# Kernel optimization log

Measured on AMD Instinct MI355X. Metric: run time of the kernel, lower is better.

The kernel has to match this reference:

```python
import jax, jax.numpy as jnp
import numpy as np

V, E = 50000, 300          # vocab, embedding dim (Word2Vec)
U1, U2, DNS = 256, 256, 128  # lstm1 units, lstm2 units, dense units
B, S = 64, 512             # batch, seq_len


def _glorot(key, shape):
    fan_in, fan_out = shape
    lim = jnp.sqrt(6.0 / (fan_in + fan_out))
    return jax.random.uniform(key, shape, jnp.float32, -lim, lim)


def setup_inputs() -> dict:
    key = jax.random.key(0)
    ks = jax.random.split(key, 12)
    d = {
        'tokens': jax.random.randint(ks[0], (B, S), 0, V),
        'emb': jax.random.normal(ks[1], (V, E), jnp.float32) * 0.05,
        # layer 1 gates: combined dim = E + U1
        'W1f': _glorot(ks[2], (E + U1, U1)), 'b1f': jnp.zeros((U1,), jnp.float32),
        'W1i': _glorot(ks[3], (E + U1, U1)), 'b1i': jnp.zeros((U1,), jnp.float32),
        'W1c': _glorot(ks[4], (E + U1, U1)), 'b1c': jnp.zeros((U1,), jnp.float32),
        'W1o': _glorot(ks[5], (E + U1, U1)), 'b1o': jnp.zeros((U1,), jnp.float32),
        # layer 2 gates: combined dim = U1 + U2
        'W2f': _glorot(ks[6], (U1 + U2, U2)), 'b2f': jnp.zeros((U2,), jnp.float32),
        'W2i': _glorot(ks[7], (U1 + U2, U2)), 'b2i': jnp.zeros((U2,), jnp.float32),
        'W2c': _glorot(ks[8], (U1 + U2, U2)), 'b2c': jnp.zeros((U2,), jnp.float32),
        'W2o': _glorot(ks[9], (U1 + U2, U2)), 'b2o': jnp.zeros((U2,), jnp.float32),
        'Wd': _glorot(ks[10], (U2, DNS)), 'bd': jnp.zeros((DNS,), jnp.float32),
        'Wout': _glorot(ks[11], (DNS, 1)), 'bout': jnp.zeros((1,), jnp.float32),
    }
    return d


def _lstm(x_seq, Wf, bf, Wi, bi, Wc, bc, Wo, bo, units):
    # x_seq: [B, S, D]; scan over time, returns all hidden states [B, S, units]
    b = x_seq.shape[0]
    h0 = jnp.zeros((b, units), x_seq.dtype)
    c0 = jnp.zeros((b, units), x_seq.dtype)

    def step(carry, x_t):
        h, c = carry
        z = jnp.concatenate([x_t, h], axis=-1)           # [B, D+units]
        f = jax.nn.sigmoid(z @ Wf + bf)
        i = jax.nn.sigmoid(z @ Wi + bi)
        g = jnp.tanh(z @ Wc + bc)
        c_new = f * c + i * g
        o = jax.nn.sigmoid(z @ Wo + bo)
        h_new = o * jnp.tanh(c_new)
        return (h_new, c_new), h_new

    (_, _), hs = jax.lax.scan(step, (h0, c0), jnp.swapaxes(x_seq, 0, 1))
    return jnp.swapaxes(hs, 0, 1)  # [B, S, units]


def reference(tokens, emb, W1f, b1f, W1i, b1i, W1c, b1c, W1o, b1o,
              W2f, b2f, W2i, b2i, W2c, b2c, W2o, b2o, Wd, bd, Wout, bout):
    x = emb[tokens]                                       # [B, S, E]
    h1 = _lstm(x, W1f, b1f, W1i, b1i, W1c, b1c, W1o, b1o, U1)   # [B, S, U1]
    h2 = _lstm(h1, W2f, b2f, W2i, b2i, W2c, b2c, W2o, b2o, U2)  # [B, S, U2]
    last = h2[:, -1, :]                                   # return_sequences=False -> final h
    d = jax.nn.relu(last @ Wd + bd)
    return jax.nn.sigmoid(d @ Wout + bout)                # [B, 1]
```

## Files before the change

kernel.cpp:

```cpp
#include <hip/hip_runtime.h>
#include <stdint.h>

typedef __bf16 bf16_t;
typedef __bf16 bf16x8 __attribute__((ext_vector_type(8)));
typedef float floatx16 __attribute__((ext_vector_type(16)));
typedef unsigned int u32;
typedef unsigned long long u64;

#define NPROD 64
#define H1R   8
#define SST   592
#define ZST   1104
#define FP    32

struct KParams {
  const int* tok;
  const float* emb;
  const float* W1[4]; const float* b1[4];
  const float* W2[4]; const float* b2[4];
  const float* Wd; const float* bd; const float* Wout; const float* bout;
  float* out;
  uint16_t* h1;
  uint16_t* h2;
  u32* fl0;
  u32* fl1;
  u32* fl0g;
  u32* pflags;
  float* dstage;
  bf16_t* w1bf;
  float* gx;
  int R;
};

__device__ __forceinline__ float sigf(float x) { return 1.f / (1.f + __expf(-x)); }
__device__ __forceinline__ float tanhf_fast(float x) { return 1.f - 2.f / (__expf(2.f * x) + 1.f); }

__device__ __forceinline__ u32 pack2(float a, float b) {
  uint16_t x = __builtin_bit_cast(uint16_t, (bf16_t)a);
  uint16_t y = __builtin_bit_cast(uint16_t, (bf16_t)b);
  return ((u32)y << 16) | (u32)x;
}
__device__ __forceinline__ float2 u2f2(u64 v) { union { u64 u; float2 f; } x; x.u = v; return x.f; }

__device__ __forceinline__ u32  ald32(const u32* p) { return __hip_atomic_load(p, __ATOMIC_RELAXED, __HIP_MEMORY_SCOPE_AGENT); }
__device__ __forceinline__ void ast32(u32* p, u32 v) { __hip_atomic_store(p, v, __ATOMIC_RELAXED, __HIP_MEMORY_SCOPE_AGENT); }
__device__ __forceinline__ u64  ald64(const u64* p) { return __hip_atomic_load(p, __ATOMIC_RELAXED, __HIP_MEMORY_SCOPE_AGENT); }

template<int NA, int NB>
__device__ __forceinline__ void waitcond(const u32* fa, u32 na, const u32* fb, u32 nb,
                                         const u32* pc, u32 nc) {
  const int lane = threadIdx.x & 63;
  const u32* ap; u32 need;
  if (lane < NA)           { ap = fa + lane * FP;        need = na; }
  else if (lane < NA + NB) { ap = fb + (lane - NA) * FP; need = nb; }
  else                     { ap = pc;                    need = nc; }
  while (!__all(ald32(ap) >= need)) {}
  __atomic_signal_fence(__ATOMIC_ACQUIRE);
}

__device__ __forceinline__ void waitg16(const u32* fa, u32 na) {
  const int lane = threadIdx.x & 63;
  const u32* ap = fa + (lane & 15) * FP;
  while (!__all(ald32(ap) >= na)) {}
  __atomic_signal_fence(__ATOMIC_ACQUIRE);
}

__device__ __forceinline__ void stage_h64(const u64* hp, char* smem) {
  const int tid = threadIdx.x;
  u64 tmp[16];
#pragma unroll
  for (int t = 0; t < 16; ++t) tmp[t] = ald64(hp + tid + 256 * t);
#pragma unroll
  for (int t = 0; t < 16; ++t) {
    int i = tid + 256 * t, b = i >> 6, cc = i & 63;
    *(u64*)(smem + b * SST + cc * 8) = tmp[t];
  }
}

__device__ void run_l0(const KParams& p, int sub, char* abuf, float* cst, float* biasl)
{
  const int tid = threadIdx.x;
  const int w = tid >> 6, l = tid & 63, q = l >> 5, lr = l & 31;
  const int mh = w & 1, nh = w >> 1;

  if (tid < 64) biasl[tid] = p.b1[tid >> 4][sub * 16 + (tid & 15)];

  const int c = nh * 32 + lr;
  const float* Wg = p.W1[c >> 4];
  const int un = sub * 16 + (c & 15);
  bf16x8 wf[16];
#pragma unroll
  for (int s = 0; s < 16; ++s)
#pragma unroll
    for (int j = 0; j < 8; ++j) {
      int k = 16 * s + 8 * q + j;
      wf[s][j] = (bf16_t)Wg[(300 + k) * 256 + un];
    }
  __syncthreads();

  float cs[2][2] = {{0.f, 0.f}, {0.f, 0.f}};

  for (int s = 0; s < 512; ++s) {
    u32 n1 = (s >= 8) ? (u32)(s - 7) : 0u;
    if (w == 0) waitcond<16, 32>(p.fl0, (u32)s, p.fl1, n1, &p.pflags[s * FP], 1u);
    __syncthreads();

    const float* slab = p.gx + (size_t)(s % p.R) * 65536u;
    u64 g[2][4];
#pragma unroll
    for (int kk = 0; kk < 2; ++kk) {
      int pp = tid + 256 * kk, b = pp >> 3, u2 = (pp & 7) * 2;
      const float* gb = slab + b * 1024 + sub * 64 + u2;
      g[kk][0] = ald64((const u64*)gb);
      g[kk][1] = ald64((const u64*)(gb + 16));
      g[kk][2] = ald64((const u64*)(gb + 32));
      g[kk][3] = ald64((const u64*)(gb + 48));
    }
    stage_h64((const u64*)(p.h1 + ((s + H1R - 1) & (H1R - 1)) * 16384), abuf);
    __syncthreads();

    floatx16 acc;
#pragma unroll
    for (int e = 0; e < 16; ++e) acc[e] = 0.f;
    const char* arow = abuf + (mh * 32 + lr) * SST + q * 16;
#pragma unroll
    for (int s2 = 0; s2 < 16; ++s2) {
      bf16x8 af = *(const bf16x8*)(arow + 32 * s2);
      acc = __builtin_amdgcn_mfma_f32_32x32x16_bf16(af, wf[s2], acc, 0, 0, 0);
    }
#pragma unroll
    for (int e = 0; e < 16; ++e) {
      int ri = (e & 3) + 8 * (e >> 2) + 4 * q;
      cst[(mh * 32 + ri) * 68 + nh * 32 + lr] = acc[e];
    }
    __syncthreads();

    uint16_t* hout = p.h1 + (s & (H1R - 1)) * 16384;
#pragma unroll
    for (int kk = 0; kk < 2; ++kk) {
      int pp = tid + 256 * kk, b = pp >> 3, u2 = (pp & 7) * 2;
      float2 pf = *(float2*)&cst[b * 68 +      u2];
      float2 pi = *(float2*)&cst[b * 68 + 16 + u2];
      float2 pg = *(float2*)&cst[b * 68 + 32 + u2];
      float2 po = *(float2*)&cst[b * 68 + 48 + u2];
      float2 gf = u2f2(g[kk][0]), gi = u2f2(g[kk][1]);
      float2 gg = u2f2(g[kk][2]), go = u2f2(g[kk][3]);
      float hv[2];
#pragma unroll
      for (int j = 0; j < 2; ++j) {
        float fj = sigf((j ? pf.y : pf.x) + (j ? gf.y : gf.x) + biasl[u2 + j]);
        float ij = sigf((j ? pi.y : pi.x) + (j ? gi.y : gi.x) + biasl[16 + u2 + j]);
        float gj = tanhf_fast((j ? pg.y : pg.x) + (j ? gg.y : gg.x) + biasl[32 + u2 + j]);
        float oj = sigf((j ? po.y : po.x) + (j ? go.y : go.x) + biasl[48 + u2 + j]);
        float cn = fj * cs[kk][j] + ij * gj;
        cs[kk][j] = cn;
        hv[j] = oj * tanhf_fast(cn);
      }
      ast32((u32*)(hout + b * 256 + sub * 16 + u2), pack2(hv[0], hv[1]));
    }
    __syncthreads();
    if (tid == 0) {
      ast32(&p.fl0[sub * FP], (u32)(s + 1));
      ast32(&p.fl0g[sub * FP], (u32)(s + 1));
    }
  }
}

__device__ void run_l1(const KParams& p, int w2, char* zbuf, float* cst, float* biasl)
{
  const int tid = threadIdx.x;
  const int wv = tid >> 6, l = tid & 63, q = l >> 5, lr = l & 31;
  const int nh = wv & 1, kh = wv >> 1;
  const int bh = w2 & 1, sub1 = w2 >> 1;

  if (tid < 64) biasl[tid] = p.b2[tid >> 4][sub1 * 16 + (tid & 15)];

  const int c = nh * 32 + lr;
  const float* Wg = p.W2[c >> 4];
  const int un = sub1 * 16 + (c & 15);
  bf16x8 wf[16];
#pragma unroll
  for (int s = 0; s < 16; ++s)
#pragma unroll
    for (int j = 0; j < 8; ++j) {
      int k = kh * 256 + s * 16 + q * 8 + j;
      wf[s][j] = (bf16_t)Wg[k * 256 + un];
    }
  __syncthreads();

  float cs2[2] = {0.f, 0.f};
  const int cb = tid >> 3, cu = (tid & 7) * 2;

  for (int s = 0; s < 512; ++s) {
    if (wv == 0) waitcond<32, 16>(p.fl1, (u32)s, p.fl0, (u32)(s + 1), p.fl0, 0u);
    __syncthreads();

    const u64* hp1 = (const u64*)(p.h1 + (s & (H1R - 1)) * 16384) + bh * 2048;
    const u64* hp2 = (const u64*)(p.h2 + ((s + 1) & 1) * 16384) + bh * 2048;
    u64 t1[8], t2[8];
#pragma unroll
    for (int t = 0; t < 8; ++t) t1[t] = ald64(hp1 + tid + 256 * t);
#pragma unroll
    for (int t = 0; t < 8; ++t) t2[t] = ald64(hp2 + tid + 256 * t);
#pragma unroll
    for (int t = 0; t < 8; ++t) {
      int i = tid + 256 * t, r = i >> 6, cc = i & 63;
      *(u64*)(zbuf + r * ZST + cc * 8) = t1[t];
    }
#pragma unroll
    for (int t = 0; t < 8; ++t) {
      int i = tid + 256 * t, r = i >> 6, cc = i & 63;
      *(u64*)(zbuf + r * ZST + 512 + cc * 8) = t2[t];
    }
    __syncthreads();

    floatx16 acc;
#pragma unroll
    for (int e = 0; e < 16; ++e) acc[e] = 0.f;
    const char* arow = zbuf + lr * ZST + kh * 512 + q * 16;
#pragma unroll
    for (int s2 = 0; s2 < 16; ++s2) {
      bf16x8 af = *(const bf16x8*)(arow + 32 * s2);
      acc = __builtin_amdgcn_mfma_f32_32x32x16_bf16(af, wf[s2], acc, 0, 0, 0);
    }
#pragma unroll
    for (int e = 0; e < 16; ++e) {
      int ri = (e & 3) + 8 * (e >> 2) + 4 * q;
      cst[kh * 2176 + ri * 68 + nh * 32 + lr] = acc[e];
    }
    __syncthreads();

    uint16_t* hout = p.h2 + (s & 1) * 16384;
    {
      float2 pf = *(float2*)&cst[cb * 68 +      cu];
      float2 pi = *(float2*)&cst[cb * 68 + 16 + cu];
      float2 pg = *(float2*)&cst[cb * 68 + 32 + cu];
      float2 po = *(float2*)&cst[cb * 68 + 48 + cu];
      float2 qf = *(float2*)&cst[2176 + cb * 68 +      cu];
      float2 qi = *(float2*)&cst[2176 + cb * 68 + 16 + cu];
      float2 qg = *(float2*)&cst[2176 + cb * 68 + 32 + cu];
      float2 qo = *(float2*)&cst[2176 + cb * 68 + 48 + cu];
      float hv[2];
#pragma unroll
      for (int j = 0; j < 2; ++j) {
        float fj = sigf((j ? pf.y + qf.y : pf.x + qf.x) + biasl[cu + j]);
        float ij = sigf((j ? pi.y + qi.y : pi.x + qi.x) + biasl[16 + cu + j]);
        float gj = tanhf_fast((j ? pg.y + qg.y : pg.x + qg.x) + biasl[32 + cu + j]);
        float oj = sigf((j ? po.y + qo.y : po.x + qo.x) + biasl[48 + cu + j]);
        float cn = fj * cs2[j] + ij * gj;
        cs2[j] = cn;
        hv[j] = oj * tanhf_fast(cn);
      }
      ast32((u32*)(hout + (bh * 32 + cb) * 256 + sub1 * 16 + cu), pack2(hv[0], hv[1]));
    }
    __syncthreads();
    if (tid == 0) ast32(&p.fl1[w2 * FP], (u32)(s + 1));
  }

  if (wv == 0) waitcond<32, 0>(p.fl1, 512u, p.fl1, 0u, p.fl1, 0u);
  __syncthreads();
  {
    const u64* hp = (const u64*)(p.h2 + 16384);
    u64 tmp[16];
#pragma unroll
    for (int t = 0; t < 16; ++t) tmp[t] = ald64(hp + tid + 256 * t);
#pragma unroll
    for (int t = 0; t < 16; ++t) {
      int i = tid + 256 * t, b = i >> 6, cc = i & 63;
      *(u64*)(zbuf + b * 520 + cc * 8) = tmp[t];
    }
  }
  __syncthreads();
  {
    int b = tid >> 2, cc = w2 * 4 + (tid & 3);
    const bf16_t* hrow = (const bf16_t*)(zbuf + b * 520);
    float a = p.bd[cc];
#pragma unroll 8
    for (int k = 0; k < 256; ++k) a += (float)hrow[k] * p.Wd[k * 128 + cc];
    ast32((u32*)&p.dstage[b * 128 + cc], __builtin_bit_cast(u32, fmaxf(a, 0.f)));
  }
  __syncthreads();
  if (tid == 0) ast32(&p.fl1[w2 * FP], 513u);

  if (w2 == 0) {
    if (wv == 0) waitcond<32, 0>(p.fl1, 513u, p.fl1, 0u, p.fl1, 0u);
    __syncthreads();
    if (tid < 64) {
      float a = p.bout[0];
#pragma unroll 8
      for (int cc = 0; cc < 128; ++cc) {
        u32 dv = ald32((u32*)&p.dstage[tid * 128 + cc]);
        a += __builtin_bit_cast(float, dv) * p.Wout[cc];
      }
      p.out[tid] = sigf(a);
    }
  }
}

__device__ void run_prod(const KParams& p, int pw, char* smem)
{
  const int tid = threadIdx.x;
  const int w = tid >> 6, l = tid & 63, q = l >> 5, lr = l & 31;
  const int mh = w & 1, chalf = w >> 1;
  const int R = p.R;

  for (int jj = 0; jj < 512 / NPROD; ++jj) {
    const int s = pw + NPROD * jj;
    if (s >= R) {
      if (w == 0) waitg16(p.fl0g, (u32)(s - R + 1));
    }
    __syncthreads();
    {
      int b = tid >> 2, qq = tid & 3;
      int tokv = p.tok[b * 512 + s];
      const float4* src = (const float4*)(p.emb + (size_t)tokv * 300);
      char* dst = smem + b * 656;
      for (int j2 = qq; j2 < 75; j2 += 4) {
        float4 v = src[j2];
        *(u32*)(dst + 8 * j2)     = pack2(v.x, v.y);
        *(u32*)(dst + 8 * j2 + 4) = pack2(v.z, v.w);
      }
      for (int i = tid; i < 640; i += 256) {
        int bb = i / 10, cc2 = i % 10;
        *(u32*)(smem + bb * 656 + 600 + cc2 * 4) = 0u;
      }
    }
    __syncthreads();

    bf16x8 afr[20];
    const char* arow = smem + (mh * 32 + lr) * 656 + q * 16;
#pragma unroll
    for (int kt = 0; kt < 20; ++kt) afr[kt] = *(const bf16x8*)(arow + 32 * kt);

    float* slab = p.gx + (size_t)(s % R) * 65536u;
    for (int c2 = 0; c2 < 16; ++c2) {
      int n = (chalf * 16 + c2) * 32 + lr;
      floatx16 acc;
#pragma unroll
      for (int e = 0; e < 16; ++e) acc[e] = 0.f;
#pragma unroll
      for (int kt = 0; kt < 20; ++kt) {
        bf16x8 bf = ((const bf16x8*)p.w1bf)[(kt * 1024 + n) * 2 + q];
        acc = __builtin_amdgcn_mfma_f32_32x32x16_bf16(afr[kt], bf, acc, 0, 0, 0);
      }
#pragma unroll
      for (int e = 0; e < 16; ++e) {
        int ri = (e & 3) + 8 * (e >> 2) + 4 * q;
        ast32((u32*)(slab + (mh * 32 + ri) * 1024 + n), __builtin_bit_cast(u32, acc[e]));
      }
    }
    __syncthreads();
    if (tid == 0) ast32(&p.pflags[s * FP], 1u);
  }
}

__global__ __launch_bounds__(256, 1) void lstm_main(KParams p)
{
  __shared__ __align__(16) char smem[64 * 656];
  __shared__ float cst[4352];
  __shared__ float biasl[64];
  const int wg = blockIdx.x;
  if (wg < 16)       run_l0(p, wg, smem, cst, biasl);
  else if (wg < 48)  run_l1(p, wg - 16, smem, cst, biasl);
  else               run_prod(p, wg - 48, smem);
}

__global__ void prep_w(KParams p) {
  int idx = blockIdx.x * 256 + threadIdx.x;
  if (idx >= 20 * 1024 * 16) return;
  int kk = idx & 15, n = (idx >> 4) & 1023, kt = idx >> 14;
  int k = kt * 16 + kk;
  int g = (n >> 4) & 3, su = n >> 6, u = n & 15;
  float v = (k < 300) ? p.W1[g][k * 256 + su * 16 + u] : 0.f;
  p.w1bf[idx] = (bf16_t)v;
}

__global__ void init_ws(u32* ws32) {
  int i = blockIdx.x * 256 + threadIdx.x;
  if (i < 100352) ws32[i] = 0u;
}

extern "C" void kernel_launch(void* const* d_in, const int* in_sizes, int n_in,
                              void* d_out, int out_size, void* d_ws, size_t ws_size,
                              hipStream_t stream)
{
  KParams p;
  p.tok = (const int*)d_in[0];
  p.emb = (const float*)d_in[1];
  for (int g = 0; g < 4; ++g) {
    p.W1[g] = (const float*)d_in[2 + 2 * g];
    p.b1[g] = (const float*)d_in[3 + 2 * g];
    p.W2[g] = (const float*)d_in[10 + 2 * g];
    p.b2[g] = (const float*)d_in[11 + 2 * g];
  }
  p.Wd   = (const float*)d_in[18];
  p.bd   = (const float*)d_in[19];
  p.Wout = (const float*)d_in[20];
  p.bout = (const float*)d_in[21];
  p.out  = (float*)d_out;

  char* ws = (char*)d_ws;
  p.h1     = (uint16_t*)ws;
  p.h2     = (uint16_t*)(ws + 262144);
  p.fl0    = (u32*)(ws + 327680);
  p.fl1    = (u32*)(ws + 329728);
  p.fl0g   = (u32*)(ws + 333824);
  p.pflags = (u32*)(ws + 335872);
  p.dstage = (float*)(ws + 401408);
  p.w1bf   = (bf16_t*)(ws + 434176);
  p.gx     = (float*)(ws + 1089536);

  long avail = (long)ws_size - 1089536L;
  int R = (int)(avail / 262144L);
  if (R > 64) R = 64;
  if (R < 1)  R = 1;
  p.R = R;

  hipLaunchKernelGGL(init_ws, dim3(392), dim3(256), 0, stream, (u32*)d_ws);
  hipLaunchKernelGGL(prep_w, dim3(1280), dim3(256), 0, stream, p);
  hipLaunchKernelGGL(lstm_main, dim3(16 + 32 + NPROD), dim3(256), 0, stream, p);
}
```

Before: 1.860 ms.

## Split LSTM batch into two halves and software-pipeline recurrence phases

Each layer's persistent workgroups now process the batch as two 32-row halves in alternating phases. While one half runs its MFMA and gate math, the hidden-state and gate-input loads for the other half are prefetched into registers, and the flag polling overlaps the MFMA work. Layer-1 is re-split so each workgroup owns 8 units across 4 K-slices with a cross-wave reduction, and per-half flags plus a larger h1 ring are added. This aims to hide global-memory latency and synchronisation on the serial recurrence critical path. The cost is more flags, more register pressure and more complex dependency tracking.

```diff
diff --git a/kernel.cpp b/kernel.cpp
--- a/kernel.cpp
+++ b/kernel.cpp
@@ -8,10 +8,12 @@
 typedef unsigned long long u64;
 
 #define NPROD 64
-#define H1R   8
+#define H1R   16
 #define SST   592
 #define ZST   1104
 #define FP    32
+
+template<int V> struct IC { static constexpr int value = V; };
 
 struct KParams {
   const int* tok;
@@ -65,161 +67,71 @@
   __atomic_signal_fence(__ATOMIC_ACQUIRE);
 }
 
-__device__ __forceinline__ void stage_h64(const u64* hp, char* smem) {
-  const int tid = threadIdx.x;
-  u64 tmp[16];
-#pragma unroll
-  for (int t = 0; t < 16; ++t) tmp[t] = ald64(hp + tid + 256 * t);
-#pragma unroll
-  for (int t = 0; t < 16; ++t) {
-    int i = tid + 256 * t, b = i >> 6, cc = i & 63;
-    *(u64*)(smem + b * SST + cc * 8) = tmp[t];
-  }
-}
-
 __device__ void run_l0(const KParams& p, int sub, char* abuf, float* cst, float* biasl)
 {
   const int tid = threadIdx.x;
   const int w = tid >> 6, l = tid & 63, q = l >> 5, lr = l & 31;
-  const int mh = w & 1, nh = w >> 1;
+  const int nh = w & 1, kh = w >> 1;
+  const int b2 = tid >> 3, u2 = (tid & 7) * 2;
 
   if (tid < 64) biasl[tid] = p.b1[tid >> 4][sub * 16 + (tid & 15)];
 
   const int c = nh * 32 + lr;
   const float* Wg = p.W1[c >> 4];
   const int un = sub * 16 + (c & 15);
-  bf16x8 wf[16];
-#pragma unroll
-  for (int s = 0; s < 16; ++s)
+  bf16x8 wf[8];
+#pragma unroll
+  for (int s2 = 0; s2 < 8; ++s2)
 #pragma unroll
     for (int j = 0; j < 8; ++j) {
-      int k = 16 * s + 8 * q + j;
-      wf[s][j] = (bf16_t)Wg[(300 + k) * 256 + un];
-    }
+      int k = kh * 128 + 16 * s2 + 8 * q + j;
+      wf[s2][j] = (bf16_t)Wg[(300 + k) * 256 + un];
+    }
+
+  float csA[2] = {0.f, 0.f}, csB[2] = {0.f, 0.f};
+  u64 rH[8], rG[4], rHn[8], rGn[4];
+
+  if (w == 0) waitcond<16, 32>(p.fl0, 0u, p.fl1, 0u, &p.pflags[0], 1u);
   __syncthreads();
-
-  float cs[2][2] = {{0.f, 0.f}, {0.f, 0.f}};
-
-  for (int s = 0; s < 512; ++s) {
-    u32 n1 = (s >= 8) ? (u32)(s - 7) : 0u;
-    if (w == 0) waitcond<16, 32>(p.fl0, (u32)s, p.fl1, n1, &p.pflags[s * FP], 1u);
-    __syncthreads();
-
-    const float* slab = p.gx + (size_t)(s % p.R) * 65536u;
-    u64 g[2][4];
-#pragma unroll
-    for (int kk = 0; kk < 2; ++kk) {
-      int pp = tid + 256 * kk, b = pp >> 3, u2 = (pp & 7) * 2;
-      const float* gb = slab + b * 1024 + sub * 64 + u2;
-      g[kk][0] = ald64((const u64*)gb);
-      g[kk][1] = ald64((const u64*)(gb + 16));
-      g[kk][2] = ald64((const u64*)(gb + 32));
-      g[kk][3] = ald64((const u64*)(gb + 48));
-    }
-    stage_h64((const u64*)(p.h1 + ((s + H1R - 1) & (H1R - 1)) * 16384), abuf);
-    __syncthreads();
-
-    floatx16 acc;
-#pragma unroll
-    for (int e = 0; e < 16; ++e) acc[e] = 0.f;
-    const char* arow = abuf + (mh * 32 + lr) * SST + q * 16;
-#pragma unroll
-    for (int s2 = 0; s2 < 16; ++s2) {
-      bf16x8 af = *(const bf16x8*)(arow + 32 * s2);
-      acc = __builtin_amdgcn_mfma_f32_32x32x16_bf16(af, wf[s2], acc, 0, 0, 0);
-    }
-#pragma unroll
-    for (int e = 0; e < 16; ++e) {
-      int ri = (e & 3) + 8 * (e >> 2) + 4 * q;
-      cst[(mh * 32 + ri) * 68 + nh * 32 + lr] = acc[e];
-    }
-    __syncthreads();
-
-    uint16_t* hout = p.h1 + (s & (H1R - 1)) * 16384;
-#pragma unroll
-    for (int kk = 0; kk < 2; ++kk) {
-      int pp = tid + 256 * kk, b = pp >> 3, u2 = (pp & 7) * 2;
-      float2 pf = *(float2*)&cst[b * 68 +      u2];
-      float2 pi = *(float2*)&cst[b * 68 + 16 + u2];
-      float2 pg = *(float2*)&cst[b * 68 + 32 + u2];
-      float2 po = *(float2*)&cst[b * 68 + 48 + u2];
-      float2 gf = u2f2(g[kk][0]), gi = u2f2(g[kk][1]);
-      float2 gg = u2f2(g[kk][2]), go = u2f2(g[kk][3]);
-      float hv[2];
-#pragma unroll
-      for (int j = 0; j < 2; ++j) {
-        float fj = sigf((j ? pf.y : pf.x) + (j ? gf.y : gf.x) + biasl[u2 + j]);
-        float ij = sigf((j ? pi.y : pi.x) + (j ? gi.y : gi.x) + biasl[16 + u2 + j]);
-        float gj = tanhf_fast((j ? pg.y : pg.x) + (j ? gg.y : gg.x) + biasl[32 + u2 + j]);
-        float oj = sigf((j ? po.y : po.x) + (j ? go.y : go.x) + biasl[48 + u2 + j]);
-        float cn = fj * cs[kk][j] + ij * gj;
-        cs[kk][j] = cn;
-        hv[j] = oj * tanhf_fast(cn);
-      }
-      ast32((u32*)(hout + b * 256 + sub * 16 + u2), pack2(hv[0], hv[1]));
-    }
-    __syncthreads();
-    if (tid == 0) {
-      ast32(&p.fl0[sub * FP], (u32)(s + 1));
-      ast32(&p.fl0g[sub * FP], (u32)(s + 1));
-    }
-  }
-}
-
-__device__ void run_l1(const KParams& p, int w2, char* zbuf, float* cst, float* biasl)
-{
-  const int tid = threadIdx.x;
-  const int wv = tid >> 6, l = tid & 63, q = l >> 5, lr = l & 31;
-  const int nh = wv & 1, kh = wv >> 1;
-  const int bh = w2 & 1, sub1 = w2 >> 1;
-
-  if (tid < 64) biasl[tid] = p.b2[tid >> 4][sub1 * 16 + (tid & 15)];
-
-  const int c = nh * 32 + lr;
-  const float* Wg = p.W2[c >> 4];
-  const int un = sub1 * 16 + (c & 15);
-  bf16x8 wf[16];
-#pragma unroll
-  for (int s = 0; s < 16; ++s)
-#pragma unroll
-    for (int j = 0; j < 8; ++j) {
-      int k = kh * 256 + s * 16 + q * 8 + j;
-      wf[s][j] = (bf16_t)Wg[k * 256 + un];
-    }
-  __syncthreads();
-
-  float cs2[2] = {0.f, 0.f};
-  const int cb = tid >> 3, cu = (tid & 7) * 2;
-
-  for (int s = 0; s < 512; ++s) {
-    if (wv == 0) waitcond<32, 16>(p.fl1, (u32)s, p.fl0, (u32)(s + 1), p.fl0, 0u);
-    __syncthreads();
-
-    const u64* hp1 = (const u64*)(p.h1 + (s & (H1R - 1)) * 16384) + bh * 2048;
-    const u64* hp2 = (const u64*)(p.h2 + ((s + 1) & 1) * 16384) + bh * 2048;
-    u64 t1[8], t2[8];
-#pragma unroll
-    for (int t = 0; t < 8; ++t) t1[t] = ald64(hp1 + tid + 256 * t);
-#pragma unroll
-    for (int t = 0; t < 8; ++t) t2[t] = ald64(hp2 + tid + 256 * t);
+  {
+    const u64* hp = (const u64*)(p.h1 + (H1R - 1) * 16384);
+#pragma unroll
+    for (int t = 0; t < 8; ++t) rH[t] = ald64(hp + tid + 256 * t);
+    const float* gb = p.gx + (size_t)b2 * 1024 + sub * 64 + u2;
+    rG[0] = ald64((const u64*)gb);
+    rG[1] = ald64((const u64*)(gb + 16));
+    rG[2] = ald64((const u64*)(gb + 32));
+    rG[3] = ald64((const u64*)(gb + 48));
+  }
+
+  auto phase = [&](auto HC, int s) {
+    constexpr int h  = decltype(HC)::value;
+    constexpr int hn = 1 - h;
+    const int sn = h ? (s + 1) : s;
+    const bool haveNext = !(h == 1 && s == 511);
+
 #pragma unroll
     for (int t = 0; t < 8; ++t) {
       int i = tid + 256 * t, r = i >> 6, cc = i & 63;
-      *(u64*)(zbuf + r * ZST + cc * 8) = t1[t];
-    }
-#pragma unroll
-    for (int t = 0; t < 8; ++t) {
-      int i = tid + 256 * t, r = i >> 6, cc = i & 63;
-      *(u64*)(zbuf + r * ZST + 512 + cc * 8) = t2[t];
-    }
-    __syncthreads();
+      *(u64*)(abuf + r * SST + cc * 8) = rH[t];
+    }
+    __syncthreads();
+
+    const u32* pollp = &p.pflags[0]; u32 need = 0u, fpre = 1u;
+    if (w == 0 && haveNext) {
+      if (l < 16)      { pollp = p.fl0 + (hn * 16 + l) * FP;        need = (u32)sn; }
+      else if (l < 48) { pollp = p.fl1 + (hn * 32 + (l - 16)) * FP;
+                         need = (sn >= H1R) ? (u32)(sn - (H1R - 1)) : 0u; }
+      else             { pollp = &p.pflags[sn * FP];                need = 1u; }
+      fpre = ald32(pollp);
+    }
 
     floatx16 acc;
 #pragma unroll
     for (int e = 0; e < 16; ++e) acc[e] = 0.f;
-    const char* arow = zbuf + lr * ZST + kh * 512 + q * 16;
-#pragma unroll
-    for (int s2 = 0; s2 < 16; ++s2) {
+    const char* arow = abuf + lr * SST + kh * 256 + q * 16;
+#pragma unroll
+    for (int s2 = 0; s2 < 8; ++s2) {
       bf16x8 af = *(const bf16x8*)(arow + 32 * s2);
       acc = __builtin_amdgcn_mfma_f32_32x32x16_bf16(af, wf[s2], acc, 0, 0, 0);
     }
@@ -228,36 +140,194 @@
       int ri = (e & 3) + 8 * (e >> 2) + 4 * q;
       cst[kh * 2176 + ri * 68 + nh * 32 + lr] = acc[e];
     }
-    __syncthreads();
-
-    uint16_t* hout = p.h2 + (s & 1) * 16384;
+    if (w == 0 && haveNext) {
+      while (!__all(fpre >= need)) fpre = ald32(pollp);
+      __atomic_signal_fence(__ATOMIC_ACQUIRE);
+    }
+    __syncthreads();
+
+    if (haveNext) {
+      const u64* hp = (const u64*)(p.h1 + ((sn + H1R - 1) & (H1R - 1)) * 16384) + hn * 2048;
+#pragma unroll
+      for (int t = 0; t < 8; ++t) rHn[t] = ald64(hp + tid + 256 * t);
+      const float* gb = p.gx + (size_t)(sn % p.R) * 65536u + (hn * 32 + b2) * 1024 + sub * 64 + u2;
+      rGn[0] = ald64((const u64*)gb);
+      rGn[1] = ald64((const u64*)(gb + 16));
+      rGn[2] = ald64((const u64*)(gb + 32));
+      rGn[3] = ald64((const u64*)(gb + 48));
+    }
+
     {
-      float2 pf = *(float2*)&cst[cb * 68 +      cu];
-      float2 pi = *(float2*)&cst[cb * 68 + 16 + cu];
-      float2 pg = *(float2*)&cst[cb * 68 + 32 + cu];
-      float2 po = *(float2*)&cst[cb * 68 + 48 + cu];
-      float2 qf = *(float2*)&cst[2176 + cb * 68 +      cu];
-      float2 qi = *(float2*)&cst[2176 + cb * 68 + 16 + cu];
-      float2 qg = *(float2*)&cst[2176 + cb * 68 + 32 + cu];
-      float2 qo = *(float2*)&cst[2176 + cb * 68 + 48 + cu];
+      float2 gf = u2f2(rG[0]), gi = u2f2(rG[1]), gg = u2f2(rG[2]), go = u2f2(rG[3]);
+      const int base = b2 * 68 + u2;
+      float2 af0 = *(float2*)&cst[base],      af1 = *(float2*)&cst[2176 + base];
+      float2 ai0 = *(float2*)&cst[base + 16], ai1 = *(float2*)&cst[2176 + base + 16];
+      float2 ag0 = *(float2*)&cst[base + 32], ag1 = *(float2*)&cst[2176 + base + 32];
+      float2 ao0 = *(float2*)&cst[base + 48], ao1 = *(float2*)&cst[2176 + base + 48];
+      float csel[2] = { h ? csB[0] : csA[0], h ? csB[1] : csA[1] };
       float hv[2];
 #pragma unroll
       for (int j = 0; j < 2; ++j) {
-        float fj = sigf((j ? pf.y + qf.y : pf.x + qf.x) + biasl[cu + j]);
-        float ij = sigf((j ? pi.y + qi.y : pi.x + qi.x) + biasl[16 + cu + j]);
-        float gj = tanhf_fast((j ? pg.y + qg.y : pg.x + qg.x) + biasl[32 + cu + j]);
-        float oj = sigf((j ? po.y + qo.y : po.x + qo.x) + biasl[48 + cu + j]);
-        float cn = fj * cs2[j] + ij * gj;
-        cs2[j] = cn;
+        float fv = j ? (af0.y + af1.y + gf.y) : (af0.x + af1.x + gf.x);
+        float iv = j ? (ai0.y + ai1.y + gi.y) : (ai0.x + ai1.x + gi.x);
+        float gv = j ? (ag0.y + ag1.y + gg.y) : (ag0.x + ag1.x + gg.x);
+        float ov = j ? (ao0.y + ao1.y + go.y) : (ao0.x + ao1.x + go.x);
+        float fj = sigf(fv + biasl[u2 + j]);
+        float ij = sigf(iv + biasl[16 + u2 + j]);
+        float gj = tanhf_fast(gv + biasl[32 + u2 + j]);
+        float oj = sigf(ov + biasl[48 + u2 + j]);
+        float cn = fj * csel[j] + ij * gj;
+        csel[j] = cn;
         hv[j] = oj * tanhf_fast(cn);
       }
-      ast32((u32*)(hout + (bh * 32 + cb) * 256 + sub1 * 16 + cu), pack2(hv[0], hv[1]));
-    }
-    __syncthreads();
-    if (tid == 0) ast32(&p.fl1[w2 * FP], (u32)(s + 1));
-  }
-
-  if (wv == 0) waitcond<32, 0>(p.fl1, 512u, p.fl1, 0u, p.fl1, 0u);
+      if (h) { csB[0] = csel[0]; csB[1] = csel[1]; }
+      else   { csA[0] = csel[0]; csA[1] = csel[1]; }
+      uint16_t* hout = p.h1 + (s & (H1R - 1)) * 16384;
+      ast32((u32*)(hout + (h * 32 + b2) * 256 + sub * 16 + u2), pack2(hv[0], hv[1]));
+    }
+    __syncthreads();
+    if (tid == 0) {
+      ast32(&p.fl0[(h * 16 + sub) * FP], (u32)(s + 1));
+      if (h == 1) ast32(&p.fl0g[sub * FP], (u32)(s + 1));
+    }
+    if (haveNext) {
+#pragma unroll
+      for (int t = 0; t < 8; ++t) rH[t] = rHn[t];
+#pragma unroll
+      for (int t = 0; t < 4; ++t) rG[t] = rGn[t];
+    }
+  };
+
+  for (int s = 0; s < 512; ++s) { phase(IC<0>{}, s); phase(IC<1>{}, s); }
+}
+
+__device__ void run_l1(const KParams& p, int wg1, char* zbuf, float* cst, float* biasl)
+{
+  const int tid = threadIdx.x;
+  const int w = tid >> 6, l = tid & 63, q = l >> 5, lr = l & 31;
+  const int kh = w;
+  const int b2 = tid >> 2, u2 = (tid & 3) * 2;
+
+  if (tid < 32) biasl[tid] = p.b2[tid >> 3][wg1 * 8 + (tid & 7)];
+
+  const float* Wg = p.W2[lr >> 3];
+  const int un = wg1 * 8 + (lr & 7);
+  bf16x8 wf[8];
+#pragma unroll
+  for (int s2 = 0; s2 < 8; ++s2)
+#pragma unroll
+    for (int j = 0; j < 8; ++j) {
+      int k = kh * 128 + 16 * s2 + 8 * q + j;
+      wf[s2][j] = (bf16_t)Wg[k * 256 + un];
+    }
+
+  float csA[2] = {0.f, 0.f}, csB[2] = {0.f, 0.f};
+  u64 r1[8], r2[8], r1n[8], r2n[8];
+
+  if (w == 0) waitcond<32, 16>(p.fl1, 0u, p.fl0, 1u, p.fl1, 0u);
+  __syncthreads();
+  {
+    const u64* hp1 = (const u64*)p.h1;
+    const u64* hp2 = (const u64*)(p.h2 + 16384);
+#pragma unroll
+    for (int t = 0; t < 8; ++t) r1[t] = ald64(hp1 + tid + 256 * t);
+#pragma unroll
+    for (int t = 0; t < 8; ++t) r2[t] = ald64(hp2 + tid + 256 * t);
+  }
+
+  auto phase = [&](auto HC, int s) {
+    constexpr int h  = decltype(HC)::value;
+    constexpr int hn = 1 - h;
+    const int sn = h ? (s + 1) : s;
+    const bool haveNext = !(h == 1 && s == 511);
+
+#pragma unroll
+    for (int t = 0; t < 8; ++t) {
+      int i = tid + 256 * t, r = i >> 6, cc = i & 63;
+      *(u64*)(zbuf + r * ZST + cc * 8) = r1[t];
+    }
+#pragma unroll
+    for (int t = 0; t < 8; ++t) {
+      int i = tid + 256 * t, r = i >> 6, cc = i & 63;
+      *(u64*)(zbuf + r * ZST + 512 + cc * 8) = r2[t];
+    }
+    __syncthreads();
+
+    const u32* pollp = p.fl1; u32 need = 0u, fpre = 1u;
+    if (w == 0 && haveNext) {
+      if (l < 32)      { pollp = p.fl1 + (hn * 32 + l) * FP;        need = (u32)sn; }
+      else if (l < 48) { pollp = p.fl0 + (hn * 16 + (l - 32)) * FP; need = (u32)(sn + 1); }
+      fpre = ald32(pollp);
+    }
+
+    floatx16 acc;
+#pragma unroll
+    for (int e = 0; e < 16; ++e) acc[e] = 0.f;
+    const char* arow = zbuf + lr * ZST + kh * 256 + q * 16;
+#pragma unroll
+    for (int s2 = 0; s2 < 8; ++s2) {
+      bf16x8 af = *(const bf16x8*)(arow + 32 * s2);
+      acc = __builtin_amdgcn_mfma_f32_32x32x16_bf16(af, wf[s2], acc, 0, 0, 0);
+    }
+#pragma unroll
+    for (int e = 0; e < 16; ++e) {
+      int ri = (e & 3) + 8 * (e >> 2) + 4 * q;
+      cst[kh * 1152 + ri * 36 + lr] = acc[e];
+    }
+    if (w == 0 && haveNext) {
+      while (!__all(fpre >= need)) fpre = ald32(pollp);
+      __atomic_signal_fence(__ATOMIC_ACQUIRE);
+    }
+    __syncthreads();
+
+    if (haveNext) {
+      const u64* hp1 = (const u64*)(p.h1 + (sn & (H1R - 1)) * 16384) + hn * 2048;
+      const u64* hp2 = (const u64*)(p.h2 + ((sn + 1) & 1) * 16384) + hn * 2048;
+#pragma unroll
+      for (int t = 0; t < 8; ++t) r1n[t] = ald64(hp1 + tid + 256 * t);
+#pragma unroll
+      for (int t = 0; t < 8; ++t) r2n[t] = ald64(hp2 + tid + 256 * t);
+    }
+
+    if (tid < 128) {
+      const int base = b2 * 36 + u2;
+      float2 vf = {0.f, 0.f}, vi = {0.f, 0.f}, vg = {0.f, 0.f}, vo = {0.f, 0.f};
+#pragma unroll
+      for (int pl = 0; pl < 4; ++pl) {
+        const float* cp = cst + pl * 1152 + base;
+        float2 a  = *(const float2*)(cp +  0); vf.x += a.x;  vf.y += a.y;
+        float2 b  = *(const float2*)(cp +  8); vi.x += b.x;  vi.y += b.y;
+        float2 g2 = *(const float2*)(cp + 16); vg.x += g2.x; vg.y += g2.y;
+        float2 o2 = *(const float2*)(cp + 24); vo.x += o2.x; vo.y += o2.y;
+      }
+      float csel[2] = { h ? csB[0] : csA[0], h ? csB[1] : csA[1] };
+      float hv[2];
+#pragma unroll
+      for (int j = 0; j < 2; ++j) {
+        float fj = sigf((j ? vf.y : vf.x) + biasl[u2 + j]);
+        float ij = sigf((j ? vi.y : vi.x) + biasl[8 + u2 + j]);
+        float gj = tanhf_fast((j ? vg.y : vg.x) + biasl[16 + u2 + j]);
+        float oj = sigf((j ? vo.y : vo.x) + biasl[24 + u2 + j]);
+        float cn = fj * csel[j] + ij * gj;
+        csel[j] = cn;
+        hv[j] = oj * tanhf_fast(cn);
+      }
+      if (h) { csB[0] = csel[0]; csB[1] = csel[1]; }
+      else   { csA[0] = csel[0]; csA[1] = csel[1]; }
+      uint16_t* hout = p.h2 + (s & 1) * 16384;
+      ast32((u32*)(hout + (h * 32 + b2) * 256 + wg1 * 8 + u2), pack2(hv[0], hv[1]));
+    }
+    __syncthreads();
+    if (tid == 0) ast32(&p.fl1[(h * 32 + wg1) * FP], (u32)(s + 1));
+    if (haveNext) {
+#pragma unroll
+      for (int t = 0; t < 8; ++t) { r1[t] = r1n[t]; r2[t] = r2n[t]; }
+    }
+  };
+
+  for (int s = 0; s < 512; ++s) { phase(IC<0>{}, s); phase(IC<1>{}, s); }
+
+  if (w == 0) waitcond<64, 0>(p.fl1, 512u, p.fl1, 0u, p.fl1, 0u);
   __syncthreads();
   {
     const u64* hp = (const u64*)(p.h2 + 16384);
@@ -272,7 +342,7 @@
   }
   __syncthreads();
   {
-    int b = tid >> 2, cc = w2 * 4 + (tid & 3);
+    int b = tid >> 2, cc = wg1 * 4 + (tid & 3);
     const bf16_t* hrow = (const bf16_t*)(zbuf + b * 520);
     float a = p.bd[cc];
 #pragma unroll 8
@@ -280,10 +350,10 @@
     ast32((u32*)&p.dstage[b * 128 + cc], __builtin_bit_cast(u32, fmaxf(a, 0.f)));
   }
   __syncthreads();
-  if (tid == 0) ast32(&p.fl1[w2 * FP], 513u);
-
-  if (w2 == 0) {
-    if (wv == 0) waitcond<32, 0>(p.fl1, 513u, p.fl1, 0u, p.fl1, 0u);
+  if (tid == 0) ast32(&p.fl1[wg1 * FP], 513u);
+
+  if (wg1 == 0) {
+    if (w == 0) waitcond<32, 0>(p.fl1, 513u, p.fl1, 0u, p.fl1, 0u);
     __syncthreads();
     if (tid < 64) {
       float a = p.bout[0];
@@ -357,7 +427,7 @@
 __global__ __launch_bounds__(256, 1) void lstm_main(KParams p)
 {
   __shared__ __align__(16) char smem[64 * 656];
-  __shared__ float cst[4352];
+  __shared__ float cst[4608];
   __shared__ float biasl[64];
   const int wg = blockIdx.x;
   if (wg < 16)       run_l0(p, wg, smem, cst, biasl);
@@ -377,7 +447,7 @@
 
 __global__ void init_ws(u32* ws32) {
   int i = blockIdx.x * 256 + threadIdx.x;
-  if (i < 100352) ws32[i] = 0u;
+  if (i < 167424) ws32[i] = 0u;
 }
 
 extern "C" void kernel_launch(void* const* d_in, const int* in_sizes, int n_in,
@@ -401,22 +471,22 @@
 
   char* ws = (char*)d_ws;
   p.h1     = (uint16_t*)ws;
-  p.h2     = (uint16_t*)(ws + 262144);
-  p.fl0    = (u32*)(ws + 327680);
-  p.fl1    = (u32*)(ws + 329728);
-  p.fl0g   = (u32*)(ws + 333824);
-  p.pflags = (u32*)(ws + 335872);
-  p.dstage = (float*)(ws + 401408);
-  p.w1bf   = (bf16_t*)(ws + 434176);
-  p.gx     = (float*)(ws + 1089536);
-
-  long avail = (long)ws_size - 1089536L;
+  p.h2     = (uint16_t*)(ws + 524288);
+  p.fl0    = (u32*)(ws + 589824);
+  p.fl1    = (u32*)(ws + 593920);
+  p.fl0g   = (u32*)(ws + 602112);
+  p.pflags = (u32*)(ws + 604160);
+  p.dstage = (float*)(ws + 669696);
+  p.w1bf   = (bf16_t*)(ws + 702464);
+  p.gx     = (float*)(ws + 1357824);
+
+  long avail = (long)ws_size - 1357824L;
   int R = (int)(avail / 262144L);
   if (R > 64) R = 64;
   if (R < 1)  R = 1;
   p.R = R;
 
-  hipLaunchKernelGGL(init_ws, dim3(392), dim3(256), 0, stream, (u32*)d_ws);
+  hipLaunchKernelGGL(init_ws, dim3(654), dim3(256), 0, stream, (u32*)d_ws);
   hipLaunchKernelGGL(prep_w, dim3(1280), dim3(256), 0, stream, p);
   hipLaunchKernelGGL(lstm_main, dim3(16 + 32 + NPROD), dim3(256), 0, stream, p);
 }
```

New measurement: 2.076 ms. +11.6%, slower.

## Replace per-block completion flags with step tags embedded in hidden-state words

Applied to the files above, without the earlier changes.

Each bf16 pair of hidden state is now stored as a 64-bit word whose upper half holds the timestep, so consumers poll the data itself instead of waiting on per-workgroup flags. This removes the trailing __syncthreads plus flag store in producers and the separate flag-wait round trip in consumers, shortening the per-step critical path of the recurrent pipeline. The cost is double the bytes for h1/h2 traffic, larger workspace, and a retry loop that re-reads entries not yet tagged.

```diff
diff --git a/kernel.cpp b/kernel.cpp
--- a/kernel.cpp
+++ b/kernel.cpp
@@ -20,9 +20,8 @@
   const float* W2[4]; const float* b2[4];
   const float* Wd; const float* bd; const float* Wout; const float* bout;
   float* out;
-  uint16_t* h1;
-  uint16_t* h2;
-  u32* fl0;
+  u64* h1;
+  u64* h2;
   u32* fl1;
   u32* fl0g;
   u32* pflags;
@@ -45,6 +44,20 @@
 __device__ __forceinline__ u32  ald32(const u32* p) { return __hip_atomic_load(p, __ATOMIC_RELAXED, __HIP_MEMORY_SCOPE_AGENT); }
 __device__ __forceinline__ void ast32(u32* p, u32 v) { __hip_atomic_store(p, v, __ATOMIC_RELAXED, __HIP_MEMORY_SCOPE_AGENT); }
 __device__ __forceinline__ u64  ald64(const u64* p) { return __hip_atomic_load(p, __ATOMIC_RELAXED, __HIP_MEMORY_SCOPE_AGENT); }
+__device__ __forceinline__ void ast64(u64* p, u64 v) { __hip_atomic_store(p, v, __ATOMIC_RELAXED, __HIP_MEMORY_SCOPE_AGENT); }
+
+template<int N>
+__device__ __forceinline__ void tag_wait(u64* tmp, const u64* hp, u32 need) {
+  const int tid = threadIdx.x;
+  bool ok = false;
+  while (!ok) {
+    ok = true;
+#pragma unroll
+    for (int t = 0; t < N; ++t)
+      if ((u32)(tmp[t] >> 32) < need) { tmp[t] = ald64(hp + tid + 256 * t); ok = false; }
+  }
+  __atomic_signal_fence(__ATOMIC_ACQUIRE);
+}
 
 template<int NA, int NB>
 __device__ __forceinline__ void waitcond(const u32* fa, u32 na, const u32* fb, u32 nb,
@@ -65,18 +78,6 @@
   __atomic_signal_fence(__ATOMIC_ACQUIRE);
 }
 
-__device__ __forceinline__ void stage_h64(const u64* hp, char* smem) {
-  const int tid = threadIdx.x;
-  u64 tmp[16];
-#pragma unroll
-  for (int t = 0; t < 16; ++t) tmp[t] = ald64(hp + tid + 256 * t);
-#pragma unroll
-  for (int t = 0; t < 16; ++t) {
-    int i = tid + 256 * t, b = i >> 6, cc = i & 63;
-    *(u64*)(smem + b * SST + cc * 8) = tmp[t];
-  }
-}
-
 __device__ void run_l0(const KParams& p, int sub, char* abuf, float* cst, float* biasl)
 {
   const int tid = threadIdx.x;
@@ -90,19 +91,20 @@
   const int un = sub * 16 + (c & 15);
   bf16x8 wf[16];
 #pragma unroll
-  for (int s = 0; s < 16; ++s)
+  for (int s2 = 0; s2 < 16; ++s2)
 #pragma unroll
     for (int j = 0; j < 8; ++j) {
-      int k = 16 * s + 8 * q + j;
-      wf[s][j] = (bf16_t)Wg[(300 + k) * 256 + un];
+      int k = 16 * s2 + 8 * q + j;
+      wf[s2][j] = (bf16_t)Wg[(300 + k) * 256 + un];
     }
   __syncthreads();
 
   float cs[2][2] = {{0.f, 0.f}, {0.f, 0.f}};
 
   for (int s = 0; s < 512; ++s) {
-    u32 n1 = (s >= 8) ? (u32)(s - 7) : 0u;
-    if (w == 0) waitcond<16, 32>(p.fl0, (u32)s, p.fl1, n1, &p.pflags[s * FP], 1u);
+    u32 n1 = (s >= H1R) ? (u32)(s - (H1R - 1)) : 0u;
+    if (w == 0) waitcond<32, 1>(p.fl1, n1, p.pflags + (size_t)s * FP, 1u,
+                                p.pflags + (size_t)s * FP, 1u);
     __syncthreads();
 
     const float* slab = p.gx + (size_t)(s % p.R) * 65536u;
@@ -116,7 +118,18 @@
       g[kk][2] = ald64((const u64*)(gb + 32));
       g[kk][3] = ald64((const u64*)(gb + 48));
     }
-    stage_h64((const u64*)(p.h1 + ((s + H1R - 1) & (H1R - 1)) * 16384), abuf);
+    {
+      const u64* hp = p.h1 + (size_t)((s + H1R - 1) & (H1R - 1)) * 8192;
+      u64 tmp[32];
+#pragma unroll
+      for (int t = 0; t < 32; ++t) tmp[t] = ald64(hp + tid + 256 * t);
+      tag_wait<32>(tmp, hp, (u32)s);
+#pragma unroll
+      for (int t = 0; t < 32; ++t) {
+        int i = tid + 256 * t, b = i >> 7, cc = i & 127;
+        *(u32*)(abuf + b * SST + cc * 4) = (u32)tmp[t];
+      }
+    }
     __syncthreads();
 
     floatx16 acc;
@@ -135,7 +148,7 @@
     }
     __syncthreads();
 
-    uint16_t* hout = p.h1 + (s & (H1R - 1)) * 16384;
+    u64* hout = p.h1 + (size_t)(s & (H1R - 1)) * 8192;
 #pragma unroll
     for (int kk = 0; kk < 2; ++kk) {
       int pp = tid + 256 * kk, b = pp >> 3, u2 = (pp & 7) * 2;
@@ -156,13 +169,10 @@
         cs[kk][j] = cn;
         hv[j] = oj * tanhf_fast(cn);
       }
-      ast32((u32*)(hout + b * 256 + sub * 16 + u2), pack2(hv[0], hv[1]));
-    }
-    __syncthreads();
-    if (tid == 0) {
-      ast32(&p.fl0[sub * FP], (u32)(s + 1));
-      ast32(&p.fl0g[sub * FP], (u32)(s + 1));
-    }
+      ast64(hout + b * 128 + sub * 8 + (u2 >> 1),
+            ((u64)(u32)(s + 1) << 32) | (u64)pack2(hv[0], hv[1]));
+    }
+    if (tid == 0) ast32(&p.fl0g[sub * FP], (u32)(s + 1));
   }
 }
 
@@ -180,11 +190,11 @@
   const int un = sub1 * 16 + (c & 15);
   bf16x8 wf[16];
 #pragma unroll
-  for (int s = 0; s < 16; ++s)
+  for (int s2 = 0; s2 < 16; ++s2)
 #pragma unroll
     for (int j = 0; j < 8; ++j) {
-      int k = kh * 256 + s * 16 + q * 8 + j;
-      wf[s][j] = (bf16_t)Wg[k * 256 + un];
+      int k = kh * 256 + s2 * 16 + q * 8 + j;
+      wf[s2][j] = (bf16_t)Wg[k * 256 + un];
     }
   __syncthreads();
 
@@ -192,25 +202,24 @@
   const int cb = tid >> 3, cu = (tid & 7) * 2;
 
   for (int s = 0; s < 512; ++s) {
-    if (wv == 0) waitcond<32, 16>(p.fl1, (u32)s, p.fl0, (u32)(s + 1), p.fl0, 0u);
-    __syncthreads();
-
-    const u64* hp1 = (const u64*)(p.h1 + (s & (H1R - 1)) * 16384) + bh * 2048;
-    const u64* hp2 = (const u64*)(p.h2 + ((s + 1) & 1) * 16384) + bh * 2048;
-    u64 t1[8], t2[8];
-#pragma unroll
-    for (int t = 0; t < 8; ++t) t1[t] = ald64(hp1 + tid + 256 * t);
-#pragma unroll
-    for (int t = 0; t < 8; ++t) t2[t] = ald64(hp2 + tid + 256 * t);
-#pragma unroll
-    for (int t = 0; t < 8; ++t) {
-      int i = tid + 256 * t, r = i >> 6, cc = i & 63;
-      *(u64*)(zbuf + r * ZST + cc * 8) = t1[t];
-    }
-#pragma unroll
-    for (int t = 0; t < 8; ++t) {
-      int i = tid + 256 * t, r = i >> 6, cc = i & 63;
-      *(u64*)(zbuf + r * ZST + 512 + cc * 8) = t2[t];
+    const u64* hp2 = p.h2 + (size_t)((s + 1) & 1) * 8192 + bh * 4096;
+    const u64* hp1 = p.h1 + (size_t)(s & (H1R - 1)) * 8192 + bh * 4096;
+    u64 t2[16], t1[16];
+#pragma unroll
+    for (int t = 0; t < 16; ++t) t2[t] = ald64(hp2 + tid + 256 * t);
+#pragma unroll
+    for (int t = 0; t < 16; ++t) t1[t] = ald64(hp1 + tid + 256 * t);
+    tag_wait<16>(t1, hp1, (u32)(s + 1));
+    tag_wait<16>(t2, hp2, (u32)s);
+#pragma unroll
+    for (int t = 0; t < 16; ++t) {
+      int i = tid + 256 * t, r = i >> 7, cc = i & 127;
+      *(u32*)(zbuf + r * ZST + cc * 4) = (u32)t1[t];
+    }
+#pragma unroll
+    for (int t = 0; t < 16; ++t) {
+      int i = tid + 256 * t, r = i >> 7, cc = i & 127;
+      *(u32*)(zbuf + r * ZST + 512 + cc * 4) = (u32)t2[t];
     }
     __syncthreads();
 
@@ -230,7 +239,6 @@
     }
     __syncthreads();
 
-    uint16_t* hout = p.h2 + (s & 1) * 16384;
     {
       float2 pf = *(float2*)&cst[cb * 68 +      cu];
       float2 pi = *(float2*)&cst[cb * 68 + 16 + cu];
@@ -251,23 +259,22 @@
         cs2[j] = cn;
         hv[j] = oj * tanhf_fast(cn);
       }
-      ast32((u32*)(hout + (bh * 32 + cb) * 256 + sub1 * 16 + cu), pack2(hv[0], hv[1]));
-    }
-    __syncthreads();
+      ast64(p.h2 + (size_t)(s & 1) * 8192 + (size_t)(bh * 32 + cb) * 128 + sub1 * 8 + (cu >> 1),
+            ((u64)(u32)(s + 1) << 32) | (u64)pack2(hv[0], hv[1]));
+    }
     if (tid == 0) ast32(&p.fl1[w2 * FP], (u32)(s + 1));
   }
 
-  if (wv == 0) waitcond<32, 0>(p.fl1, 512u, p.fl1, 0u, p.fl1, 0u);
-  __syncthreads();
   {
-    const u64* hp = (const u64*)(p.h2 + 16384);
-    u64 tmp[16];
-#pragma unroll
-    for (int t = 0; t < 16; ++t) tmp[t] = ald64(hp + tid + 256 * t);
-#pragma unroll
-    for (int t = 0; t < 16; ++t) {
-      int i = tid + 256 * t, b = i >> 6, cc = i & 63;
-      *(u64*)(zbuf + b * 520 + cc * 8) = tmp[t];
+    const u64* hp = p.h2 + 8192;
+    u64 tmp[32];
+#pragma unroll
+    for (int t = 0; t < 32; ++t) tmp[t] = ald64(hp + tid + 256 * t);
+    tag_wait<32>(tmp, hp, 512u);
+#pragma unroll
+    for (int t = 0; t < 32; ++t) {
+      int i = tid + 256 * t, b = i >> 7, cc = i & 127;
+      *(u32*)(zbuf + b * 520 + cc * 4) = (u32)tmp[t];
     }
   }
   __syncthreads();
@@ -377,7 +384,7 @@
 
 __global__ void init_ws(u32* ws32) {
   int i = blockIdx.x * 256 + threadIdx.x;
-  if (i < 100352) ws32[i] = 0u;
+  if (i < 181760) ws32[i] = 0u;
 }
 
 extern "C" void kernel_launch(void* const* d_in, const int* in_sizes, int n_in,
@@ -400,23 +407,22 @@
   p.out  = (float*)d_out;
 
   char* ws = (char*)d_ws;
-  p.h1     = (uint16_t*)ws;
-  p.h2     = (uint16_t*)(ws + 262144);
-  p.fl0    = (u32*)(ws + 327680);
-  p.fl1    = (u32*)(ws + 329728);
-  p.fl0g   = (u32*)(ws + 333824);
-  p.pflags = (u32*)(ws + 335872);
-  p.dstage = (float*)(ws + 401408);
-  p.w1bf   = (bf16_t*)(ws + 434176);
-  p.gx     = (float*)(ws + 1089536);
-
-  long avail = (long)ws_size - 1089536L;
+  p.h1     = (u64*)ws;
+  p.h2     = (u64*)(ws + 524288);
+  p.fl1    = (u32*)(ws + 655360);
+  p.fl0g   = (u32*)(ws + 659456);
+  p.pflags = (u32*)(ws + 661504);
+  p.dstage = (float*)(ws + 727040);
+  p.w1bf   = (bf16_t*)(ws + 759808);
+  p.gx     = (float*)(ws + 1415168);
+
+  long avail = (long)ws_size - 1415168L;
   int R = (int)(avail / 262144L);
   if (R > 64) R = 64;
   if (R < 1)  R = 1;
   p.R = R;
 
-  hipLaunchKernelGGL(init_ws, dim3(392), dim3(256), 0, stream, (u32*)d_ws);
+  hipLaunchKernelGGL(init_ws, dim3(710), dim3(256), 0, stream, (u32*)d_ws);
   hipLaunchKernelGGL(prep_w, dim3(1280), dim3(256), 0, stream, p);
   hipLaunchKernelGGL(lstm_main, dim3(16 + 32 + NPROD), dim3(256), 0, stream, p);
 }
```

Result: slower. 2.441 ms (+31.2%).
